# Kernel tuning notes

Hardware: AMD Instinct MI355X
Metric: run time of the kernel (lower is better)

## Reference

```python
import jax, jax.numpy as jnp
import numpy as np

INPUT_SIZE = 512
HIDDEN_SIZE = 512
BATCH = 64
SEQ_LEN = 512


def _xavier(key, shape):
    fan_in, fan_out = shape[0], shape[1]
    limit = float(np.sqrt(6.0 / (fan_in + fan_out)))
    return jax.random.uniform(key, shape, jnp.float32, -limit, limit)


def setup_inputs() -> dict:
    key = jax.random.key(0)
    ks = jax.random.split(key, 14)
    inp = {
        "inputs": jax.random.normal(ks[0], (BATCH, SEQ_LEN, INPUT_SIZE), jnp.float32),
        "W_i": _xavier(ks[1], (INPUT_SIZE, HIDDEN_SIZE)),
        "W_f": _xavier(ks[2], (INPUT_SIZE, HIDDEN_SIZE)),
        "W_o": _xavier(ks[3], (INPUT_SIZE, HIDDEN_SIZE)),
        "W_c": _xavier(ks[4], (INPUT_SIZE, HIDDEN_SIZE)),
        "U_i": _xavier(ks[5], (HIDDEN_SIZE, HIDDEN_SIZE)),
        "U_f": _xavier(ks[6], (HIDDEN_SIZE, HIDDEN_SIZE)),
        "U_o": _xavier(ks[7], (HIDDEN_SIZE, HIDDEN_SIZE)),
        "U_c": _xavier(ks[8], (HIDDEN_SIZE, HIDDEN_SIZE)),
        "b_i": _xavier(ks[9], (1, HIDDEN_SIZE)),
        "b_f": _xavier(ks[10], (1, HIDDEN_SIZE)),
        "b_o": _xavier(ks[11], (1, HIDDEN_SIZE)),
        "b_c": _xavier(ks[12], (1, HIDDEN_SIZE)),
    }
    return inp


def reference(inputs, W_i, W_f, W_o, W_c, U_i, U_f, U_o, U_c, b_i, b_f, b_o, b_c):
    B, S, D = inputs.shape
    H = W_i.shape[1]
    # Fuse the 4 input projections into one GEMM over the whole sequence
    # (same math as per-step separate matmuls, just batched).
    W = jnp.concatenate([W_i, W_f, W_o, W_c], axis=1)      # [D, 4H]
    U = jnp.concatenate([U_i, U_f, U_o, U_c], axis=1)      # [H, 4H]
    b = jnp.concatenate([b_i, b_f, b_o, b_c], axis=1)      # [1, 4H]
    x_proj = jnp.einsum('bsd,dg->sbg', inputs, W) + b      # [S, B, 4H]

    def step(carry, xp):
        h, c = carry
        gates = xp + h @ U                                  # [B, 4H]
        i_g = jax.nn.sigmoid(gates[:, 0*H:1*H])
        f_g = jax.nn.sigmoid(gates[:, 1*H:2*H])
        o_g = jax.nn.sigmoid(gates[:, 2*H:3*H])
        c_t = jnp.tanh(gates[:, 3*H:4*H])
        c_new = f_g * c + i_g * c_t
        h_new = o_g * jnp.tanh(c_new)
        return (h_new, c_new), None

    h0 = jnp.zeros((B, H), jnp.float32)
    c0 = jnp.zeros((B, H), jnp.float32)
    (h_final, _), _ = jax.lax.scan(step, (h0, c0), x_proj)
    return h_final
```

## Files before the change

kernel.cpp:

```cpp
#include <hip/hip_runtime.h>


#define NG   4
#define GR   16
#define NS   32
#define SC   16
#define DIM  512
#define HID  512
#define SEQ  512
#define NTHR 256
#define NWG  (NG*NS)

#define AOFF 0
#define GOFF (GR*1024)
#define BOFF (GOFF + 4096)
#define LDS_BYTES (BOFF + 64*2048)

#define WS_FLAG_BYTES 16384
#define HBUF_UINTS   (2*NG*GR*256)
#define WS_NEED      (WS_FLAG_BYTES + HBUF_UINTS*4)

typedef float f32x4  __attribute__((ext_vector_type(4)));
typedef short bf16x8 __attribute__((ext_vector_type(8)));

__device__ __forceinline__ unsigned short f2bf(float f){
  union { float f; unsigned u; } v; v.f = f;
  unsigned r = v.u + 0x7fffu + ((v.u >> 16) & 1u);
  return (unsigned short)(r >> 16);
}
__device__ __forceinline__ float sigm(float x){ return 1.0f/(1.0f + __expf(-x)); }
__device__ __forceinline__ float tanh_f(float x){
  float e = __expf(-2.0f * fabsf(x));
  float t = (1.0f - e)/(1.0f + e);
  return x < 0.0f ? -t : t;
}

__global__ void zero_ws_kernel(uint4* p, int n4){
  int i = blockIdx.x*blockDim.x + threadIdx.x;
  uint4 z; z.x=0u; z.y=0u; z.z=0u; z.w=0u;
  if (i < n4) p[i] = z;
}

__global__ __launch_bounds__(NTHR, 1) void lstm_persistent(
  const float* __restrict__ x,
  const float* __restrict__ W0, const float* __restrict__ W1,
  const float* __restrict__ W2, const float* __restrict__ W3,
  const float* __restrict__ U0, const float* __restrict__ U1,
  const float* __restrict__ U2, const float* __restrict__ U3,
  const float* __restrict__ b0, const float* __restrict__ b1,
  const float* __restrict__ b2, const float* __restrict__ b3,
  float* __restrict__ out,
  unsigned* __restrict__ flags,
  unsigned* __restrict__ hbuf32)
{
  __shared__ __align__(16) char smem[LDS_BYTES];
  const int tid = threadIdx.x;
  const int bid = blockIdx.x;
  const int g = bid >> 5;
  const int s = bid & 31;
  const int w = tid >> 6;
  const int l = tid & 63;

  {
    const int q  = tid & 3;
    const int kk = tid >> 2;
    for (int gate = 0; gate < 4; ++gate){
      const float* Wsrc = (gate==0)?W0:(gate==1)?W1:(gate==2)?W2:W3;
      const float* Usrc = (gate==0)?U0:(gate==1)?U1:(gate==2)?U2:U3;
      #pragma unroll
      for (int kb = 0; kb < 16; ++kb){
        const int k = kb*64 + kk;
        const float* p = (k < DIM)
          ? (Wsrc + (size_t)k*HID + s*SC + q*4)
          : (Usrc + (size_t)(k-DIM)*HID + s*SC + q*4);
        f32x4 v = *(const f32x4*)p;
        #pragma unroll
        for (int j = 0; j < 4; ++j){
          const int c = gate*16 + q*4 + j;
          const unsigned byte = ((unsigned)(k*2)) ^ ((unsigned)((c&7)<<4));
          *(unsigned short*)(&smem[BOFF + c*2048] + byte) = f2bf(v[j]);
        }
      }
    }
  }

  const int er = tid >> 4;
  const int ec = tid & 15;
  const int ecol = s*SC + ec;
  const float bi = b0[ecol], bff = b1[ecol], bo = b2[ecol], bc = b3[ecol];
  float cstate = 0.0f, hout = 0.0f;

  const int arow = l & 15;
  const int qh   = l >> 4;
  const unsigned swz = (unsigned)((arow & 7) << 4);
  const char* Abase = &smem[AOFF + arow*1024];
  const char* Bbase = &smem[BOFF + (w*16 + arow)*2048];
  float* gatesLds = (float*)&smem[GOFF];

  const int sr  = tid >> 4;
  const int sdb = tid & 15;
  const unsigned swzS = (unsigned)((sr & 7) << 4);
  char* Arow = &smem[AOFF + sr*1024];

  unsigned* gflags = flags + g*1024;

#define STAGE_X(T) do { \
    const float* xp = x + ((size_t)(g*GR + sr)*SEQ + (size_t)(T))*DIM + sdb*32; \
    _Pragma("unroll") \
    for (int j = 0; j < 4; ++j){ \
      f32x4 u = *(const f32x4*)(xp + j*8); \
      f32x4 v = *(const f32x4*)(xp + j*8 + 4); \
      bf16x8 o8; \
      o8[0]=(short)f2bf(u[0]); o8[1]=(short)f2bf(u[1]); \
      o8[2]=(short)f2bf(u[2]); o8[3]=(short)f2bf(u[3]); \
      o8[4]=(short)f2bf(v[0]); o8[5]=(short)f2bf(v[1]); \
      o8[6]=(short)f2bf(v[2]); o8[7]=(short)f2bf(v[3]); \
      *(bf16x8*)(Arow + (((unsigned)(sdb*64 + j*16)) ^ swzS)) = o8; \
    } \
  } while(0)

#define GEMM_STEP(QA, QB, ACC) do { \
    bf16x8 a_ = *(const bf16x8*)(Abase + (((unsigned)((QA)*64 + qh*16)) ^ swz)); \
    bf16x8 b_ = *(const bf16x8*)(Bbase + (((unsigned)((QB)*64 + qh*16)) ^ swz)); \
    ACC = __builtin_amdgcn_mfma_f32_16x16x32_bf16(a_, b_, ACC, 0, 0, 0); \
  } while(0)

  STAGE_X(0);

  for (int t = 0; t < SEQ; ++t){
    __syncthreads();

    f32x4 acc0 = {0.f,0.f,0.f,0.f}, acc1 = {0.f,0.f,0.f,0.f};
    f32x4 acc2 = {0.f,0.f,0.f,0.f}, acc3 = {0.f,0.f,0.f,0.f};

    #pragma unroll
    for (int q4 = 0; q4 < 4; ++q4){
      GEMM_STEP(q4*4+0, q4*4+0, acc0);
      GEMM_STEP(q4*4+1, q4*4+1, acc1);
      GEMM_STEP(q4*4+2, q4*4+2, acc2);
      GEMM_STEP(q4*4+3, q4*4+3, acc3);
    }

    if (t > 0 && tid < 32){
      const unsigned* fp = &gflags[tid*32];
      while (__hip_atomic_load(fp, __ATOMIC_RELAXED, __HIP_MEMORY_SCOPE_AGENT)
             < (unsigned)t) { }
    }
    __syncthreads();

    {
      const unsigned* hsrc =
        hbuf32 + ((size_t)((t&1)*NG + g)*GR + sr)*256 + sdb*16;
      unsigned ld[16];
      #pragma unroll
      for (int j = 0; j < 16; ++j)
        ld[j] = __hip_atomic_load(hsrc + j, __ATOMIC_RELAXED,
                                  __HIP_MEMORY_SCOPE_AGENT);
      #pragma unroll
      for (int q = 0; q < 4; ++q){
        bf16x8 o;
        #pragma unroll
        for (int e = 0; e < 4; ++e){
          unsigned u = ld[q*4 + e];
          o[2*e]   = (short)(u & 0xffffu);
          o[2*e+1] = (short)(u >> 16);
        }
        *(bf16x8*)(Arow + (((unsigned)(sdb*64 + q*16)) ^ swzS)) = o;
      }
    }
    __syncthreads();

    #pragma unroll
    for (int q4 = 0; q4 < 4; ++q4){
      GEMM_STEP(q4*4+0, q4*4+16, acc0);
      GEMM_STEP(q4*4+1, q4*4+17, acc1);
      GEMM_STEP(q4*4+2, q4*4+18, acc2);
      GEMM_STEP(q4*4+3, q4*4+19, acc3);
    }

    f32x4 accs = (acc0 + acc1) + (acc2 + acc3);
    #pragma unroll
    for (int rr = 0; rr < 4; ++rr)
      gatesLds[(qh*4 + rr)*64 + w*16 + arow] = accs[rr];
    __syncthreads();

    {
      float gi = gatesLds[er*64 +  0 + ec] + bi;
      float gf = gatesLds[er*64 + 16 + ec] + bff;
      float go = gatesLds[er*64 + 32 + ec] + bo;
      float gc = gatesLds[er*64 + 48 + ec] + bc;
      float ig = sigm(gi), fg = sigm(gf), og = sigm(go), ct = tanh_f(gc);
      cstate = fg*cstate + ig*ct;
      hout = og * tanh_f(cstate);
      unsigned hb = (unsigned)f2bf(hout);
      unsigned ob = __shfl_xor(hb, 1);
      if ((tid & 1) == 0){
        unsigned val = hb | (ob << 16);
        unsigned idx = (unsigned)((((t+1)&1)*NG + g)*GR + er)*256u
                     + (unsigned)(s*8 + (ec>>1));
        __hip_atomic_store(hbuf32 + idx, val, __ATOMIC_RELAXED,
                           __HIP_MEMORY_SCOPE_AGENT);
      }
    }

    if (t + 1 < SEQ) STAGE_X(t+1);

    __syncthreads();

    if (tid == 0)
      __hip_atomic_store(&gflags[s*32], (unsigned)(t+1),
                         __ATOMIC_RELAXED, __HIP_MEMORY_SCOPE_AGENT);
  }

  out[(size_t)(g*GR + er)*HID + s*SC + ec] = hout;
#undef GEMM_STEP
#undef STAGE_X
}

extern "C" void kernel_launch(void* const* d_in, const int* in_sizes, int n_in,
                              void* d_out, int out_size, void* d_ws, size_t ws_size,
                              hipStream_t stream)
{
  (void)in_sizes; (void)n_in; (void)out_size;
  if (ws_size < (size_t)WS_NEED) return;

  const float* x  = (const float*)d_in[0];
  const float* W0 = (const float*)d_in[1];
  const float* W1 = (const float*)d_in[2];
  const float* W2 = (const float*)d_in[3];
  const float* W3 = (const float*)d_in[4];
  const float* U0 = (const float*)d_in[5];
  const float* U1 = (const float*)d_in[6];
  const float* U2 = (const float*)d_in[7];
  const float* U3 = (const float*)d_in[8];
  const float* b0 = (const float*)d_in[9];
  const float* b1 = (const float*)d_in[10];
  const float* b2 = (const float*)d_in[11];
  const float* b3 = (const float*)d_in[12];
  float* out = (float*)d_out;

  unsigned* flags  = (unsigned*)d_ws;
  unsigned* hbuf32 = (unsigned*)((char*)d_ws + WS_FLAG_BYTES);

  const int n4 = WS_NEED / 16;
  zero_ws_kernel<<<dim3((n4 + 255)/256), dim3(256), 0, stream>>>((uint4*)d_ws, n4);
  lstm_persistent<<<dim3(NWG), dim3(NTHR), 0, stream>>>(
      x, W0,W1,W2,W3, U0,U1,U2,U3, b0,b1,b2,b3, out, flags, hbuf32);
}
```

Baseline: 2.824 ms.

## Reorder LSTM step to prefetch x into registers and overlap h loads with x-GEMM

Each timestep is reordered so the flag wait and the global h loads come first. The h loads are kept in registers while the x tile is converted and the x-part MFMA runs, then h is written to LDS for the recurrent GEMM. The next step's x row is now prefetched into registers rather than converted and stored to LDS at the end of the step, and the recurrent GEMM is skipped at t=0. This is meant to hide h-load latency behind the x GEMM. In exchange, the x GEMM no longer runs during the cross-workgroup flag wait, and each step has more barriers.

```diff
diff --git a/kernel.cpp b/kernel.cpp
--- a/kernel.cpp
+++ b/kernel.cpp
@@ -22,6 +22,8 @@
 
 typedef float f32x4  __attribute__((ext_vector_type(4)));
 typedef short bf16x8 __attribute__((ext_vector_type(8)));
+
+union HPack { unsigned u[4]; bf16x8 v; };
 
 __device__ __forceinline__ unsigned short f2bf(float f){
   union { float f; unsigned u; } v; v.f = f;
@@ -103,21 +105,11 @@
   char* Arow = &smem[AOFF + sr*1024];
 
   unsigned* gflags = flags + g*1024;
-
-#define STAGE_X(T) do { \
-    const float* xp = x + ((size_t)(g*GR + sr)*SEQ + (size_t)(T))*DIM + sdb*32; \
-    _Pragma("unroll") \
-    for (int j = 0; j < 4; ++j){ \
-      f32x4 u = *(const f32x4*)(xp + j*8); \
-      f32x4 v = *(const f32x4*)(xp + j*8 + 4); \
-      bf16x8 o8; \
-      o8[0]=(short)f2bf(u[0]); o8[1]=(short)f2bf(u[1]); \
-      o8[2]=(short)f2bf(u[2]); o8[3]=(short)f2bf(u[3]); \
-      o8[4]=(short)f2bf(v[0]); o8[5]=(short)f2bf(v[1]); \
-      o8[6]=(short)f2bf(v[2]); o8[7]=(short)f2bf(v[3]); \
-      *(bf16x8*)(Arow + (((unsigned)(sdb*64 + j*16)) ^ swzS)) = o8; \
-    } \
-  } while(0)
+  const float* xrow = x + (size_t)(g*GR + sr)*SEQ*DIM + sdb*32;
+  const unsigned* hrow_base = hbuf32 + (size_t)(g*GR + sr)*256 + sdb*16;
+
+  f32x4 xr[8];
+  HPack hp[4];
 
 #define GEMM_STEP(QA, QB, ACC) do { \
     bf16x8 a_ = *(const bf16x8*)(Abase + (((unsigned)((QA)*64 + qh*16)) ^ swz)); \
@@ -125,9 +117,43 @@
     ACC = __builtin_amdgcn_mfma_f32_16x16x32_bf16(a_, b_, ACC, 0, 0, 0); \
   } while(0)
 
-  STAGE_X(0);
+  {
+    const float* xp = xrow;
+    #pragma unroll
+    for (int j = 0; j < 8; ++j) xr[j] = *(const f32x4*)(xp + j*4);
+  }
+
+  __syncthreads();
 
   for (int t = 0; t < SEQ; ++t){
+    if (t > 0 && tid < 32){
+      const unsigned* fp = &gflags[tid*32];
+      while (__hip_atomic_load(fp, __ATOMIC_RELAXED, __HIP_MEMORY_SCOPE_AGENT)
+             < (unsigned)t) { }
+    }
+    __syncthreads();
+
+    if (t > 0){
+      const unsigned* hsrc = hrow_base + (size_t)((t&1)*NG)*GR*256;
+      #pragma unroll
+      for (int j = 0; j < 4; ++j){
+        #pragma unroll
+        for (int e = 0; e < 4; ++e)
+          hp[j].u[e] = __hip_atomic_load(hsrc + j*4 + e, __ATOMIC_RELAXED,
+                                         __HIP_MEMORY_SCOPE_AGENT);
+      }
+    }
+
+    #pragma unroll
+    for (int j = 0; j < 4; ++j){
+      f32x4 u = xr[2*j], v = xr[2*j+1];
+      bf16x8 o8;
+      o8[0]=(short)f2bf(u[0]); o8[1]=(short)f2bf(u[1]);
+      o8[2]=(short)f2bf(u[2]); o8[3]=(short)f2bf(u[3]);
+      o8[4]=(short)f2bf(v[0]); o8[5]=(short)f2bf(v[1]);
+      o8[6]=(short)f2bf(v[2]); o8[7]=(short)f2bf(v[3]);
+      *(bf16x8*)(Arow + (((unsigned)(sdb*64 + j*16)) ^ swzS)) = o8;
+    }
     __syncthreads();
 
     f32x4 acc0 = {0.f,0.f,0.f,0.f}, acc1 = {0.f,0.f,0.f,0.f};
@@ -140,42 +166,23 @@
       GEMM_STEP(q4*4+2, q4*4+2, acc2);
       GEMM_STEP(q4*4+3, q4*4+3, acc3);
     }
-
-    if (t > 0 && tid < 32){
-      const unsigned* fp = &gflags[tid*32];
-      while (__hip_atomic_load(fp, __ATOMIC_RELAXED, __HIP_MEMORY_SCOPE_AGENT)
-             < (unsigned)t) { }
-    }
-    __syncthreads();
-
-    {
-      const unsigned* hsrc =
-        hbuf32 + ((size_t)((t&1)*NG + g)*GR + sr)*256 + sdb*16;
-      unsigned ld[16];
-      #pragma unroll
-      for (int j = 0; j < 16; ++j)
-        ld[j] = __hip_atomic_load(hsrc + j, __ATOMIC_RELAXED,
-                                  __HIP_MEMORY_SCOPE_AGENT);
-      #pragma unroll
-      for (int q = 0; q < 4; ++q){
-        bf16x8 o;
-        #pragma unroll
-        for (int e = 0; e < 4; ++e){
-          unsigned u = ld[q*4 + e];
-          o[2*e]   = (short)(u & 0xffffu);
-          o[2*e+1] = (short)(u >> 16);
-        }
-        *(bf16x8*)(Arow + (((unsigned)(sdb*64 + q*16)) ^ swzS)) = o;
-      }
-    }
-    __syncthreads();
-
-    #pragma unroll
-    for (int q4 = 0; q4 < 4; ++q4){
-      GEMM_STEP(q4*4+0, q4*4+16, acc0);
-      GEMM_STEP(q4*4+1, q4*4+17, acc1);
-      GEMM_STEP(q4*4+2, q4*4+18, acc2);
-      GEMM_STEP(q4*4+3, q4*4+19, acc3);
+    __syncthreads();
+
+    if (t > 0){
+      #pragma unroll
+      for (int j = 0; j < 4; ++j)
+        *(bf16x8*)(Arow + (((unsigned)(sdb*64 + j*16)) ^ swzS)) = hp[j].v;
+    }
+    __syncthreads();
+
+    if (t > 0){
+      #pragma unroll
+      for (int q4 = 0; q4 < 4; ++q4){
+        GEMM_STEP(q4*4+0, q4*4+16, acc0);
+        GEMM_STEP(q4*4+1, q4*4+17, acc1);
+        GEMM_STEP(q4*4+2, q4*4+18, acc2);
+        GEMM_STEP(q4*4+3, q4*4+19, acc3);
+      }
     }
 
     f32x4 accs = (acc0 + acc1) + (acc2 + acc3);
@@ -202,10 +209,14 @@
                            __HIP_MEMORY_SCOPE_AGENT);
       }
     }
-
-    if (t + 1 < SEQ) STAGE_X(t+1);
-
-    __syncthreads();
+    __syncthreads();
+
+    {
+      const int tn = (t + 1 < SEQ) ? (t + 1) : t;
+      const float* xp = xrow + (size_t)tn*DIM;
+      #pragma unroll
+      for (int j = 0; j < 8; ++j) xr[j] = *(const f32x4*)(xp + j*4);
+    }
 
     if (tid == 0)
       __hip_atomic_store(&gflags[s*32], (unsigned)(t+1),
@@ -214,7 +225,6 @@
 
   out[(size_t)(g*GR + er)*HID + s*SC + ec] = hout;
 #undef GEMM_STEP
-#undef STAGE_X
 }
 
 extern "C" void kernel_launch(void* const* d_in, const int* in_sizes, int n_in,
```

Result: slower. 2.977 ms (+5.4%).
